# Optimization experiments

Measured on AMD Instinct MI355X. Metric: run time of the kernel, lower is better.

The kernel has to match this reference:

```python
import jax, jax.numpy as jnp
import numpy as np

SQRT3 = 1.7320508075688772
SQRT3_2 = 0.8660254037844386
SQRT3_3 = 0.5773502691896257

N_POINTS = 8388608
CAM_RINGS = 24      # hex camera rings -> 3*R^2+3*R+1 = 1801 pixels
KERNEL_RINGS = 1    # splat stencil rings -> 7 neighbor offsets
SIGMA = 0.5


def _build_sensor():
    """Precompute the static (eqx.field(static=True)) sensor geometry, faithfully
    reproducing _detect_hex_grid / _build_lookup_table / _hex_neighbor_offsets."""
    R = CAM_RINGS
    qs = [(q, r) for q in range(-R, R + 1) for r in range(-R, R + 1)
          if max(abs(q), abs(r), abs(q + r)) <= R]
    q = np.array([a for a, _ in qs], np.float64)
    r = np.array([b for _, b in qs], np.float64)
    centers = np.stack([SQRT3 * (q + r / 2.0), 1.5 * r], axis=1)  # pointy-top, size=1
    n = len(centers)
    # _detect_hex_grid
    diff = centers[:, None, :] - centers[None, :, :]
    dist_sq = (diff ** 2).sum(-1)
    np.fill_diagonal(dist_sq, np.inf)
    min_dist = np.sqrt(dist_sq.min())
    i, j = np.unravel_index(np.argmin(dist_sq), dist_sq.shape)
    vec = centers[i] - centers[j]
    rot = float(np.mod(np.arctan2(vec[1], vec[0]), np.pi / 3.0))
    offset = centers[np.argmin((centers ** 2).sum(1))]
    hex_size = float(min_dist / SQRT3)
    # _build_lookup_table
    xs = centers[:, 0] - offset[0]
    ys = centers[:, 1] - offset[1]
    c, s = np.cos(-rot), np.sin(-rot)
    xr = c * xs - s * ys
    yr = s * xs + c * ys
    qf = (SQRT3_3 * xr - yr / 3.0) / hex_size
    rf = 2.0 * yr / 3.0 / hex_size
    qi = np.round(qf).astype(np.int32)
    ri = np.round(rf).astype(np.int32)
    q_min, r_min = int(qi.min()), int(ri.min())
    table = np.full((int(qi.max()) - q_min + 1, int(ri.max()) - r_min + 1), -1, np.int32)
    table[qi - q_min, ri - r_min] = np.arange(n, dtype=np.int32)
    # _hex_neighbor_offsets
    K = KERNEL_RINGS
    offs = [(a, b) for a in range(-K, K + 1) for b in range(-K, K + 1)
            if max(abs(a), abs(b), abs(a + b)) <= K]
    nq = np.array([o[0] for o in offs], np.int32)
    nr = np.array([o[1] for o in offs], np.int32)
    ox = (hex_size * SQRT3 * (nq + nr / 2.0)).astype(np.float32)
    oy = (hex_size * 1.5 * nr).astype(np.float32)
    return dict(
        lookup_table=jnp.asarray(table),
        neighbor_q=jnp.asarray(nq), neighbor_r=jnp.asarray(nr),
        neighbor_ox=jnp.asarray(ox), neighbor_oy=jnp.asarray(oy),
        hex_size=hex_size, hex_inradius=hex_size * SQRT3_2,
        grid_rotation=rot, grid_offset=(float(offset[0]), float(offset[1])),
        q_min=q_min, r_min=r_min, n_pixels=n,
    )

SENSOR = _build_sensor()


def _axial_round(q, r):
    s = -q - r
    qi, ri, si = jnp.round(q), jnp.round(r), jnp.round(s)
    dq, dr, ds = jnp.abs(qi - q), jnp.abs(ri - r), jnp.abs(si - s)
    qi = jnp.where((dq > dr) & (dq > ds), -ri - si, qi)
    ri = jnp.where((dr > dq) & (dr > ds), -qi - si, ri)
    return qi, ri


def setup_inputs() -> dict:
    key = jax.random.key(0)
    k1, k2, k3 = jax.random.split(key, 3)
    # camera footprint half-extent ~ SQRT3*CAM_RINGS; sample mostly inside
    L = 0.6 * SQRT3 * CAM_RINGS
    x = jax.random.uniform(k1, (N_POINTS,), jnp.float32, -L, L)
    y = jax.random.uniform(k2, (N_POINTS,), jnp.float32, -L, L)
    values = jax.random.normal(k3, (N_POINTS,), jnp.float32)
    return {"x": x, "y": y, "values": values}


def reference(x, y, values):
    S = SENSOR
    hs = S["hex_size"]
    inr = S["hex_inradius"]
    # rotate into grid frame by -grid_rotation
    c = jnp.cos(-S["grid_rotation"]).astype(x.dtype) if False else np.float32(np.cos(-S["grid_rotation"]))
    s = np.float32(np.sin(-S["grid_rotation"]))
    xs = x - np.float32(S["grid_offset"][0])
    ys = y - np.float32(S["grid_offset"][1])
    x_g = c * xs - s * ys
    y_g = s * xs + c * ys
    # cartesian -> fractional axial -> nearest hex center
    q = (SQRT3_3 * x_g - y_g / 3.0) / hs
    r = 2.0 * y_g / 3.0 / hs
    q_base, r_base = _axial_round(q, r)
    base_x = hs * SQRT3 * (q_base + r_base / 2.0)
    base_y = hs * 1.5 * r_base
    dx = x_g - base_x
    dy = y_g - base_y
    # neighbor stencil: [P, 7]
    qi = q_base[:, None].astype(jnp.int32) + S["neighbor_q"]
    ri = r_base[:, None].astype(jnp.int32) + S["neighbor_r"]
    dist_x = dx[:, None] - S["neighbor_ox"]
    dist_y = dy[:, None] - S["neighbor_oy"]
    hex_dist = jnp.maximum(jnp.abs(dist_y),
                           SQRT3_2 * jnp.abs(dist_x) + 0.5 * jnp.abs(dist_y)) / inr
    weights = jnp.exp(-0.5 * (hex_dist / SIGMA) ** 2)
    weights = weights / weights.sum(axis=1, keepdims=True)
    # lookup-table gather with bounds masking
    tbl = S["lookup_table"]
    q_idx = qi - S["q_min"]
    r_idx = ri - S["r_min"]
    in_bounds = (q_idx >= 0) & (q_idx < tbl.shape[0]) & (r_idx >= 0) & (r_idx < tbl.shape[1])
    q_safe = jnp.clip(q_idx, 0, tbl.shape[0] - 1)
    r_safe = jnp.clip(r_idx, 0, tbl.shape[1] - 1)
    pixel_idx = tbl[q_safe, r_safe]
    valid = in_bounds & (pixel_idx >= 0)
    pixel_idx = jnp.where(valid, pixel_idx, 0)
    splatted = values[:, None] * weights * valid
    return jax.ops.segment_sum(splatted.reshape(-1), pixel_idx.reshape(-1),
                               num_segments=S["n_pixels"])
```

## Files before the change

kernel.cpp:

```cpp
#include <hip/hip_runtime.h>
#include <hip/hip_bf16.h>

#define NPIX 1801
#define NT   256
#define NB   4096
#define MAXSLICES 32

#define FXSCALE 1048576.0f
#define FXINV   (1.0f / 1048576.0f)
#define KHD 1.9614249f
#define KHX 1.6986438f

#if __has_builtin(__builtin_amdgcn_exp2f)
#define EXP2F(x) __builtin_amdgcn_exp2f(x)
#else
#define EXP2F(x) __expf((x) * 0.69314718f)
#endif

#if __has_builtin(__builtin_amdgcn_rcpf)
#define RCPF(x) __builtin_amdgcn_rcpf(x)
#else
#define RCPF(x) (1.0f / (x))
#endif

__device__ __forceinline__ int col_base(int q) {
    int a = q + 24;
    return (q <= 0) ? (a * 26 + ((a * (a - 1)) >> 1))
                    : (900 + 49 * q - ((q * (q - 1)) >> 1));
}

__device__ __forceinline__ bool in_hex(int q, int r) {
    return (unsigned)(q + 24) <= 48u && (unsigned)(r + 24) <= 48u &&
           (unsigned)(q + r + 24) <= 48u;
}

__global__ __launch_bounds__(NT) void hexsplat_kernel(
    const float* __restrict__ xs, const float* __restrict__ ys,
    const float* __restrict__ vs, unsigned int* __restrict__ acc,
    int n4, int slice_mask)
{
    __shared__ unsigned int hist[2 * NPIX];
    #pragma unroll 4
    for (int i = threadIdx.x; i < 2 * NPIX; i += NT) hist[i] = 0u;
    __syncthreads();

    const int pbase = (threadIdx.x & 1) ? NPIX : 0;
    const int tid = blockIdx.x * NT + threadIdx.x;
    const int stride = NB * NT;
    const float4* x4 = (const float4*)xs;
    const float4* y4 = (const float4*)ys;
    const float4* v4 = (const float4*)vs;

    for (int i = tid; i < n4; i += stride) {
        float4 xq = x4[i];
        float4 yq = y4[i];
        float4 vq = v4[i];
        #pragma unroll
        for (int k = 0; k < 4; ++k) {
            float px = (&xq.x)[k];
            float py = (&yq.x)[k];
            float pv = (&vq.x)[k];

            float q = fmaf(-0.33333334f, py, 0.57735027f * px);
            float r = 0.66666669f * py;

            float sn = -q - r;
            float qi = rintf(q), ri = rintf(r), si = rintf(sn);
            float dq = fabsf(qi - q), dr = fabsf(ri - r), ds = fabsf(si - sn);
            if (dq > dr && dq > ds)      qi = -ri - si;
            else if (dr > dq && dr > ds) ri = -qi - si;

            int qb = (int)qi;
            int rb = (int)ri;

            float dx = fmaf(-1.7320508f, fmaf(0.5f, ri, qi), px);
            float dy = fmaf(-1.5f, ri, py);

            float dm = dy - 1.5f,        dp = dy + 1.5f;
            float em = dx - 0.8660254f,  ep = dx + 0.8660254f;
            float eM = dx - 1.7320508f,  eP = dx + 1.7320508f;
            float c0 = KHD * fabsf(dy), cm = KHD * fabsf(dm), cp = KHD * fabsf(dp);
            float h0 = 0.5f * c0,       hm = 0.5f * cm,       hp = 0.5f * cp;
            float u0 = fmaxf(c0, fmaf(KHX, fabsf(eP), h0));
            float u1 = fmaxf(cm, fmaf(KHX, fabsf(ep), hm));
            float u2 = fmaxf(cp, fmaf(KHX, fabsf(ep), hp));
            float u3 = fmaxf(c0, fmaf(KHX, fabsf(dx), h0));
            float u4 = fmaxf(cm, fmaf(KHX, fabsf(em), hm));
            float u5 = fmaxf(cp, fmaf(KHX, fabsf(em), hp));
            float u6 = fmaxf(c0, fmaf(KHX, fabsf(eM), h0));
            float w0 = EXP2F(-(u0 * u0));
            float w1 = EXP2F(-(u1 * u1));
            float w2 = EXP2F(-(u2 * u2));
            float w3 = EXP2F(-(u3 * u3));
            float w4 = EXP2F(-(u4 * u4));
            float w5 = EXP2F(-(u5 * u5));
            float w6 = EXP2F(-(u6 * u6));
            float wsum = ((w0 + w1) + (w2 + w3)) + ((w4 + w5) + w6);
            float vinv = (pv * FXSCALE) * RCPF(wsum);

            bool interior = ((unsigned)(qb + 23) <= 46u) &
                            ((unsigned)(rb + 23) <= 46u) &
                            ((unsigned)(qb + rb + 23) <= 46u);
            if (interior) {
                int m  = qb < 0 ? -qb : qb;
                int t  = (m * (99 - m)) >> 1;
                int b1 = 900 + rb + pbase + (qb < 0 ? -t : t);
                int t2 = qb + qb;
                int a0 = t2 - 1; a0 = a0 < 0 ? -a0 : a0;
                int a2 = t2 + 1; a2 = a2 < 0 ? -a2 : a2;
                int A0 = b1 - ((99 - a0) >> 1);
                int A2 = b1 + ((99 - a2) >> 1);
                atomicAdd(&hist[A0],     (unsigned int)(int)(w0 * vinv));
                atomicAdd(&hist[A0 + 1], (unsigned int)(int)(w1 * vinv));
                atomicAdd(&hist[b1 - 1], (unsigned int)(int)(w2 * vinv));
                atomicAdd(&hist[b1],     (unsigned int)(int)(w3 * vinv));
                atomicAdd(&hist[b1 + 1], (unsigned int)(int)(w4 * vinv));
                atomicAdd(&hist[A2 - 1], (unsigned int)(int)(w5 * vinv));
                atomicAdd(&hist[A2],     (unsigned int)(int)(w6 * vinv));
            } else {
                const int nq_[7] = {-1, -1, 0, 0, 0, 1, 1};
                const int nr_[7] = {0, 1, -1, 0, 1, -1, 0};
                float warr[7] = {w0, w1, w2, w3, w4, w5, w6};
                #pragma unroll
                for (int nn = 0; nn < 7; ++nn) {
                    int qn = qb + nq_[nn];
                    int rn = rb + nr_[nn];
                    if (in_hex(qn, rn)) {
                        atomicAdd(&hist[col_base(qn) + rn + pbase],
                                  (unsigned int)(int)(warr[nn] * vinv));
                    }
                }
            }
        }
    }

    __syncthreads();
    unsigned int* aslice = acc + (size_t)(blockIdx.x & slice_mask) * NPIX;
    for (int i = threadIdx.x; i < NPIX; i += NT) {
        atomicAdd(&aslice[i], hist[i] + hist[i + NPIX]);
    }
}

__global__ void finalize_kernel(const unsigned int* __restrict__ acc,
                                float* __restrict__ out, int nslices)
{
    int i = blockIdx.x * blockDim.x + threadIdx.x;
    if (i < NPIX) {
        unsigned int s = 0;
        for (int k = 0; k < nslices; ++k) s += acc[(size_t)k * NPIX + i];
        out[i] = (float)(int)s * FXINV;
    }
}

extern "C" void kernel_launch(void* const* d_in, const int* in_sizes, int n_in,
                              void* d_out, int out_size, void* d_ws, size_t ws_size,
                              hipStream_t stream) {
    const float* x = (const float*)d_in[0];
    const float* y = (const float*)d_in[1];
    const float* v = (const float*)d_in[2];
    float* out = (float*)d_out;
    unsigned int* acc = (unsigned int*)d_ws;
    int n = in_sizes[0];
    int n4 = n / 4;

    int nslices = 1;
    while (nslices < MAXSLICES &&
           (size_t)(nslices * 2) * NPIX * sizeof(unsigned int) <= ws_size)
        nslices *= 2;

    hipMemsetAsync(acc, 0, (size_t)nslices * NPIX * sizeof(unsigned int), stream);
    hexsplat_kernel<<<NB, NT, 0, stream>>>(x, y, v, acc, n4, nslices - 1);
    finalize_kernel<<<(NPIX + 255) / 256, 256, 0, stream>>>(acc, out, nslices);
}
```

Measured before the change: 137.2 us.

## Use single shared histogram, hoist loads for exact-size input, simplify weight math

Drops the duplicated per-parity shared histogram for a single copy, which halves the shared-memory footprint and the flush work but may raise LDS atomic contention. Adds a specialized path for the case where the input is exactly two float4s per thread, loading both up front so memory latency overlaps with compute. Pre-scales dx/dy so the hex-distance terms use fewer FMAs, moves the interior test to float compares, and marks the interior branch as likely.

```diff
diff --git a/kernel.cpp b/kernel.cpp
--- a/kernel.cpp
+++ b/kernel.cpp
@@ -9,19 +9,9 @@
 #define FXSCALE 1048576.0f
 #define FXINV   (1.0f / 1048576.0f)
 #define KHD 1.9614249f
-#define KHX 1.6986438f
-
-#if __has_builtin(__builtin_amdgcn_exp2f)
-#define EXP2F(x) __builtin_amdgcn_exp2f(x)
-#else
-#define EXP2F(x) __expf((x) * 0.69314718f)
-#endif
-
-#if __has_builtin(__builtin_amdgcn_rcpf)
-#define RCPF(x) __builtin_amdgcn_rcpf(x)
-#else
-#define RCPF(x) (1.0f / (x))
-#endif
+#define KHX 1.6986436f
+#define C1  1.4710687f
+#define C2  2.9421374f
 
 __device__ __forceinline__ int col_base(int q) {
     int a = q + 24;
@@ -34,110 +24,121 @@
            (unsigned)(q + r + 24) <= 48u;
 }
 
+__device__ __forceinline__ void splat_point(float px, float py, float pv,
+                                            unsigned int* hist)
+{
+    float q = fmaf(-0.33333334f, py, 0.57735027f * px);
+    float r = 0.66666669f * py;
+
+    float sn = -q - r;
+    float qi = rintf(q), ri = rintf(r), si = rintf(sn);
+    float dq = fabsf(qi - q), dr = fabsf(ri - r), ds = fabsf(si - sn);
+    if (dq > dr && dq > ds)      qi = -ri - si;
+    else if (dr > dq && dr > ds) ri = -qi - si;
+
+    int qb = (int)qi;
+    int rb = (int)ri;
+
+    float dx = fmaf(-1.7320508f, fmaf(0.5f, ri, qi), px);
+    float dy = fmaf(-1.5f, ri, py);
+
+    float Y  = KHD * dy;
+    float X  = KHX * dx;
+    float Ym = Y - C2, Yp = Y + C2;
+    float Xm = X - C1, Xp = X + C1;
+    float XM = X - C2, XP = X + C2;
+    float h0 = 0.5f * fabsf(Y);
+    float hm = 0.5f * fabsf(Ym);
+    float hp = 0.5f * fabsf(Yp);
+    float u0 = fmaxf(fabsf(Y),  fabsf(XP) + h0);
+    float u1 = fmaxf(fabsf(Ym), fabsf(Xp) + hm);
+    float u2 = fmaxf(fabsf(Yp), fabsf(Xp) + hp);
+    float u3 = fmaxf(fabsf(Y),  fabsf(X)  + h0);
+    float u4 = fmaxf(fabsf(Ym), fabsf(Xm) + hm);
+    float u5 = fmaxf(fabsf(Yp), fabsf(Xm) + hp);
+    float u6 = fmaxf(fabsf(Y),  fabsf(XM) + h0);
+    float w0 = __builtin_amdgcn_exp2f(-(u0 * u0));
+    float w1 = __builtin_amdgcn_exp2f(-(u1 * u1));
+    float w2 = __builtin_amdgcn_exp2f(-(u2 * u2));
+    float w3 = __builtin_amdgcn_exp2f(-(u3 * u3));
+    float w4 = __builtin_amdgcn_exp2f(-(u4 * u4));
+    float w5 = __builtin_amdgcn_exp2f(-(u5 * u5));
+    float w6 = __builtin_amdgcn_exp2f(-(u6 * u6));
+    float wsum = ((w0 + w1) + (w2 + w3)) + ((w4 + w5) + w6);
+    float vinv = (pv * FXSCALE) * __builtin_amdgcn_rcpf(wsum);
+
+    bool interior = (fabsf(qi) <= 23.0f) & (fabsf(ri) <= 23.0f) &
+                    (fabsf(qi + ri) <= 23.0f);
+    if (__builtin_expect(interior, 1)) {
+        int m  = qb < 0 ? -qb : qb;
+        int t  = (m * (99 - m)) >> 1;
+        int b1 = 900 + rb + (qb < 0 ? -t : t);
+        int t2 = qb + qb;
+        int a0 = t2 - 1; a0 = a0 < 0 ? -a0 : a0;
+        int a2 = t2 + 1; a2 = a2 < 0 ? -a2 : a2;
+        int A0 = b1 - ((99 - a0) >> 1);
+        int A2 = b1 + ((99 - a2) >> 1);
+        atomicAdd(&hist[A0],     (unsigned int)(int)(w0 * vinv));
+        atomicAdd(&hist[A0 + 1], (unsigned int)(int)(w1 * vinv));
+        atomicAdd(&hist[b1 - 1], (unsigned int)(int)(w2 * vinv));
+        atomicAdd(&hist[b1],     (unsigned int)(int)(w3 * vinv));
+        atomicAdd(&hist[b1 + 1], (unsigned int)(int)(w4 * vinv));
+        atomicAdd(&hist[A2 - 1], (unsigned int)(int)(w5 * vinv));
+        atomicAdd(&hist[A2],     (unsigned int)(int)(w6 * vinv));
+    } else {
+        const int nq_[7] = {-1, -1, 0, 0, 0, 1, 1};
+        const int nr_[7] = {0, 1, -1, 0, 1, -1, 0};
+        float warr[7] = {w0, w1, w2, w3, w4, w5, w6};
+        #pragma unroll
+        for (int nn = 0; nn < 7; ++nn) {
+            int qn = qb + nq_[nn];
+            int rn = rb + nr_[nn];
+            if (in_hex(qn, rn)) {
+                atomicAdd(&hist[col_base(qn) + rn],
+                          (unsigned int)(int)(warr[nn] * vinv));
+            }
+        }
+    }
+}
+
 __global__ __launch_bounds__(NT) void hexsplat_kernel(
     const float* __restrict__ xs, const float* __restrict__ ys,
     const float* __restrict__ vs, unsigned int* __restrict__ acc,
     int n4, int slice_mask)
 {
-    __shared__ unsigned int hist[2 * NPIX];
+    __shared__ unsigned int hist[NPIX];
     #pragma unroll 4
-    for (int i = threadIdx.x; i < 2 * NPIX; i += NT) hist[i] = 0u;
+    for (int i = threadIdx.x; i < NPIX; i += NT) hist[i] = 0u;
     __syncthreads();
 
-    const int pbase = (threadIdx.x & 1) ? NPIX : 0;
-    const int tid = blockIdx.x * NT + threadIdx.x;
-    const int stride = NB * NT;
+    const int t0 = blockIdx.x * NT + threadIdx.x;
     const float4* x4 = (const float4*)xs;
     const float4* y4 = (const float4*)ys;
     const float4* v4 = (const float4*)vs;
 
-    for (int i = tid; i < n4; i += stride) {
-        float4 xq = x4[i];
-        float4 yq = y4[i];
-        float4 vq = v4[i];
+    if (n4 == 2 * NB * NT) {
+        const int t1 = t0 + NB * NT;
+        float4 xa = x4[t0], ya = y4[t0], va = v4[t0];
+        float4 xb = x4[t1], yb = y4[t1], vb = v4[t1];
         #pragma unroll
-        for (int k = 0; k < 4; ++k) {
-            float px = (&xq.x)[k];
-            float py = (&yq.x)[k];
-            float pv = (&vq.x)[k];
-
-            float q = fmaf(-0.33333334f, py, 0.57735027f * px);
-            float r = 0.66666669f * py;
-
-            float sn = -q - r;
-            float qi = rintf(q), ri = rintf(r), si = rintf(sn);
-            float dq = fabsf(qi - q), dr = fabsf(ri - r), ds = fabsf(si - sn);
-            if (dq > dr && dq > ds)      qi = -ri - si;
-            else if (dr > dq && dr > ds) ri = -qi - si;
-
-            int qb = (int)qi;
-            int rb = (int)ri;
-
-            float dx = fmaf(-1.7320508f, fmaf(0.5f, ri, qi), px);
-            float dy = fmaf(-1.5f, ri, py);
-
-            float dm = dy - 1.5f,        dp = dy + 1.5f;
-            float em = dx - 0.8660254f,  ep = dx + 0.8660254f;
-            float eM = dx - 1.7320508f,  eP = dx + 1.7320508f;
-            float c0 = KHD * fabsf(dy), cm = KHD * fabsf(dm), cp = KHD * fabsf(dp);
-            float h0 = 0.5f * c0,       hm = 0.5f * cm,       hp = 0.5f * cp;
-            float u0 = fmaxf(c0, fmaf(KHX, fabsf(eP), h0));
-            float u1 = fmaxf(cm, fmaf(KHX, fabsf(ep), hm));
-            float u2 = fmaxf(cp, fmaf(KHX, fabsf(ep), hp));
-            float u3 = fmaxf(c0, fmaf(KHX, fabsf(dx), h0));
-            float u4 = fmaxf(cm, fmaf(KHX, fabsf(em), hm));
-            float u5 = fmaxf(cp, fmaf(KHX, fabsf(em), hp));
-            float u6 = fmaxf(c0, fmaf(KHX, fabsf(eM), h0));
-            float w0 = EXP2F(-(u0 * u0));
-            float w1 = EXP2F(-(u1 * u1));
-            float w2 = EXP2F(-(u2 * u2));
-            float w3 = EXP2F(-(u3 * u3));
-            float w4 = EXP2F(-(u4 * u4));
-            float w5 = EXP2F(-(u5 * u5));
-            float w6 = EXP2F(-(u6 * u6));
-            float wsum = ((w0 + w1) + (w2 + w3)) + ((w4 + w5) + w6);
-            float vinv = (pv * FXSCALE) * RCPF(wsum);
-
-            bool interior = ((unsigned)(qb + 23) <= 46u) &
-                            ((unsigned)(rb + 23) <= 46u) &
-                            ((unsigned)(qb + rb + 23) <= 46u);
-            if (interior) {
-                int m  = qb < 0 ? -qb : qb;
-                int t  = (m * (99 - m)) >> 1;
-                int b1 = 900 + rb + pbase + (qb < 0 ? -t : t);
-                int t2 = qb + qb;
-                int a0 = t2 - 1; a0 = a0 < 0 ? -a0 : a0;
-                int a2 = t2 + 1; a2 = a2 < 0 ? -a2 : a2;
-                int A0 = b1 - ((99 - a0) >> 1);
-                int A2 = b1 + ((99 - a2) >> 1);
-                atomicAdd(&hist[A0],     (unsigned int)(int)(w0 * vinv));
-                atomicAdd(&hist[A0 + 1], (unsigned int)(int)(w1 * vinv));
-                atomicAdd(&hist[b1 - 1], (unsigned int)(int)(w2 * vinv));
-                atomicAdd(&hist[b1],     (unsigned int)(int)(w3 * vinv));
-                atomicAdd(&hist[b1 + 1], (unsigned int)(int)(w4 * vinv));
-                atomicAdd(&hist[A2 - 1], (unsigned int)(int)(w5 * vinv));
-                atomicAdd(&hist[A2],     (unsigned int)(int)(w6 * vinv));
-            } else {
-                const int nq_[7] = {-1, -1, 0, 0, 0, 1, 1};
-                const int nr_[7] = {0, 1, -1, 0, 1, -1, 0};
-                float warr[7] = {w0, w1, w2, w3, w4, w5, w6};
-                #pragma unroll
-                for (int nn = 0; nn < 7; ++nn) {
-                    int qn = qb + nq_[nn];
-                    int rn = rb + nr_[nn];
-                    if (in_hex(qn, rn)) {
-                        atomicAdd(&hist[col_base(qn) + rn + pbase],
-                                  (unsigned int)(int)(warr[nn] * vinv));
-                    }
-                }
-            }
+        for (int k = 0; k < 4; ++k)
+            splat_point((&xa.x)[k], (&ya.x)[k], (&va.x)[k], hist);
+        #pragma unroll
+        for (int k = 0; k < 4; ++k)
+            splat_point((&xb.x)[k], (&yb.x)[k], (&vb.x)[k], hist);
+    } else {
+        for (int i = t0; i < n4; i += NB * NT) {
+            float4 xq = x4[i], yq = y4[i], vq = v4[i];
+            #pragma unroll
+            for (int k = 0; k < 4; ++k)
+                splat_point((&xq.x)[k], (&yq.x)[k], (&vq.x)[k], hist);
         }
     }
 
     __syncthreads();
     unsigned int* aslice = acc + (size_t)(blockIdx.x & slice_mask) * NPIX;
     for (int i = threadIdx.x; i < NPIX; i += NT) {
-        atomicAdd(&aslice[i], hist[i] + hist[i + NPIX]);
+        atomicAdd(&aslice[i], hist[i]);
     }
 }
 
```

After: 137.3 us. Within noise of the previous version (+0.1%).
